# Kernel tuning notes

Hardware: AMD Instinct MI355X
Metric: run time of the kernel (lower is better)

## Reference

```python
import jax, jax.numpy as jnp
import numpy as np

B, D, H, NB = 16384, 1024, 256, 16

def setup_inputs() -> dict:
    key = jax.random.key(0)
    ks = jax.random.split(key, 10)
    s_d = 1.0 / np.sqrt(D)
    s_h = 1.0 / np.sqrt(H)
    return {
        "x":   jax.random.normal(ks[0], (B, D), jnp.float32),
        # switch: Linear(D,H) -> relu -> Linear(H, 3*NB)
        "Ws1": jax.random.normal(ks[1], (D, H), jnp.float32) * s_d,
        "bs1": jnp.zeros((H,), jnp.float32),
        "Ws2": jax.random.normal(ks[2], (H, 3 * NB), jnp.float32) * s_h,
        "bs2": jnp.zeros((3 * NB,), jnp.float32),
        # per-branch bottleneck FC operators: D -> H -> D
        "W1":  jax.random.normal(ks[3], (NB, D, H), jnp.float32) * s_d,
        "b1":  jnp.zeros((NB, H), jnp.float32),
        "W2":  jax.random.normal(ks[4], (NB, H, D), jnp.float32) * s_h,
        "b2":  jnp.zeros((NB, D), jnp.float32),
        # noise: uniform for gumbel, normal for reparameterized gaussian
        "u":   jax.random.uniform(ks[5], (B, NB), jnp.float32, 1e-6, 1.0 - 1e-6),
        "eps": jax.random.normal(ks[6], (B, NB), jnp.float32),
    }

def reference(x, Ws1, bs1, Ws2, bs2, W1, b1, W2, b2, u, eps):
    # switch -> control signals, reshaped to (B, 3, NB)
    ctrl = jax.nn.relu(x @ Ws1 + bs1) @ Ws2 + bs2
    ctrl = ctrl.reshape(-1, 3, NB)
    y_logits, z_mean, z_logvar = ctrl[:, 0], ctrl[:, 1], ctrl[:, 2]

    # gumbel-softmax sample (tau = 1)
    g = -jnp.log(-jnp.log(u))
    y = jax.nn.softmax(y_logits + g, axis=-1)          # soft sample (B, NB)
    y_idx = jnp.argmax(y, axis=-1)                     # hard branch per sample

    # gaussian reparameterization
    z = z_mean + jnp.exp(0.5 * z_logvar) * eps         # (B, NB)

    # per-branch bottleneck FC, z of the branch gates the bottleneck
    h = jax.nn.relu(jnp.einsum('bd,ndh->bnh', x, W1) + b1)   # (B, NB, H)
    h = h * z[:, :, None]
    o = jnp.einsum('bnh,nhd->bnd', h, W2) + b2               # (B, NB, D)

    # combine: keep only the branch selected by y_idx
    onehot = jax.nn.one_hot(y_idx, NB, dtype=x.dtype)        # (B, NB)
    out = jnp.einsum('bnd,bn->bd', o, onehot)                # (B, D)

    return (x + out, y_logits, y_idx, y, z_mean, z_logvar, z)
```

## Files before the change

### kernel.cpp

```cpp
#include <hip/hip_runtime.h>
#include <hip/hip_bf16.h>
#include <stdint.h>

#define Bn 16384
#define Dd 1024
#define Hh 256
#define NBk 16

#define O1 ((size_t)Bn*Dd)
#define O2 (O1 + (size_t)Bn*NBk)
#define O3 (O2 + (size_t)Bn)
#define O4 (O3 + (size_t)Bn*NBk)
#define O5 (O4 + (size_t)Bn*NBk)
#define O6 (O5 + (size_t)Bn*NBk)

typedef __attribute__((ext_vector_type(8))) short s16x8;
typedef __attribute__((ext_vector_type(4))) float f32x4;

#define MFMA_BF16(a,b,c) __builtin_amdgcn_mfma_f32_16x16x32_bf16((a),(b),(c),0,0,0)

__device__ __forceinline__ float blo(unsigned v){ return __uint_as_float(v << 16); }
__device__ __forceinline__ float bhi(unsigned v){ return __uint_as_float(v & 0xFFFF0000u); }
__device__ __forceinline__ unsigned short f2b(float f){
  unsigned u = __float_as_uint(f);
  return (unsigned short)((u + 0x7FFFu + ((u >> 16) & 1u)) >> 16);
}
__device__ __forceinline__ s16x8 cvt8(const f32x4 u0, const f32x4 u1) {
  s16x8 v;
  v[0]=(short)f2b(u0[0]); v[1]=(short)f2b(u0[1]); v[2]=(short)f2b(u0[2]); v[3]=(short)f2b(u0[3]);
  v[4]=(short)f2b(u1[0]); v[5]=(short)f2b(u1[1]); v[6]=(short)f2b(u1[2]); v[7]=(short)f2b(u1[3]);
  return v;
}
__device__ __forceinline__ void split8(const f32x4 u0, const f32x4 u1, s16x8& hi, s16x8& lo) {
  #pragma unroll
  for (int e = 0; e < 4; ++e) {
    const unsigned short h = f2b(u0[e]);
    hi[e] = (short)h;
    lo[e] = (short)f2b(u0[e] - __uint_as_float((unsigned)h << 16));
  }
  #pragma unroll
  for (int e = 0; e < 4; ++e) {
    const unsigned short h = f2b(u1[e]);
    hi[4+e] = (short)h;
    lo[4+e] = (short)f2b(u1[e] - __uint_as_float((unsigned)h << 16));
  }
}
__device__ __forceinline__ void gload16(const void* g, void* lds) {
  __builtin_amdgcn_global_load_lds(
      (const __attribute__((address_space(1))) unsigned int*)g,
      (__attribute__((address_space(3))) unsigned int*)lds, 16, 0, 0);
}

__global__ __launch_bounds__(256) void kA1(const float* __restrict__ x, const float* __restrict__ Ws1,
                                           const float* __restrict__ bs1, float* __restrict__ A1)
{
  const int b0 = blockIdx.x * 64;
  const int c0 = blockIdx.y * 128;
  __shared__ float XS[32][68];
  __shared__ float WS[32][128];
  const int tid = threadIdx.x;
  const int ty = tid >> 4, tx = tid & 15;
  float acc[4][8];
  #pragma unroll
  for (int r = 0; r < 4; ++r)
    #pragma unroll
    for (int c = 0; c < 8; ++c) acc[r][c] = 0.f;

  for (int k0 = 0; k0 < Dd; k0 += 32) {
    #pragma unroll
    for (int it = 0; it < 2; ++it) {
      int i = tid + 256*it;
      int row = i >> 3, kq = i & 7;
      float4 v = *(const float4*)&x[(size_t)(b0+row)*Dd + k0 + 4*kq];
      XS[4*kq+0][row] = v.x; XS[4*kq+1][row] = v.y; XS[4*kq+2][row] = v.z; XS[4*kq+3][row] = v.w;
    }
    #pragma unroll
    for (int it = 0; it < 4; ++it) {
      int i = tid + 256*it;
      int k = i >> 5, cq = i & 31;
      *(float4*)&WS[k][4*cq] = *(const float4*)&Ws1[(size_t)(k0+k)*Hh + c0 + 4*cq];
    }
    __syncthreads();
    #pragma unroll
    for (int k = 0; k < 32; ++k) {
      const float4 xv = *(const float4*)&XS[k][ty*4];
      const float4 w0 = *(const float4*)&WS[k][tx*4];
      const float4 w1 = *(const float4*)&WS[k][tx*4+64];
      const float xr[4] = {xv.x, xv.y, xv.z, xv.w};
      const float wr[8] = {w0.x,w0.y,w0.z,w0.w,w1.x,w1.y,w1.z,w1.w};
      #pragma unroll
      for (int r = 0; r < 4; ++r)
        #pragma unroll
        for (int c = 0; c < 8; ++c)
          acc[r][c] = fmaf(xr[r], wr[c], acc[r][c]);
    }
    __syncthreads();
  }
  const float4 bv0 = *(const float4*)&bs1[c0 + tx*4];
  const float4 bv1 = *(const float4*)&bs1[c0 + tx*4 + 64];
  const float br[8] = {bv0.x,bv0.y,bv0.z,bv0.w,bv1.x,bv1.y,bv1.z,bv1.w};
  #pragma unroll
  for (int r = 0; r < 4; ++r) {
    int row = b0 + ty*4 + r;
    float o[8];
    #pragma unroll
    for (int c = 0; c < 8; ++c) o[c] = fmaxf(acc[r][c] + br[c], 0.f);
    float4 s0 = {o[0],o[1],o[2],o[3]};
    float4 s1 = {o[4],o[5],o[6],o[7]};
    *(float4*)&A1[(size_t)row*Hh + c0 + tx*4]      = s0;
    *(float4*)&A1[(size_t)row*Hh + c0 + tx*4 + 64] = s1;
  }
}

__global__ __launch_bounds__(256) void kTW(const float* __restrict__ in,
                                           unsigned short* __restrict__ hi,
                                           unsigned short* __restrict__ lo)
{
  const int i0 = blockIdx.x * 32, j0 = blockIdx.y * 32;
  __shared__ float T[32][33];
  const int t = threadIdx.x;
  {
    const int ii = t >> 3, jj = (t & 7) * 4;
    float4 v = *(const float4*)&in[(size_t)(i0+ii)*Hh + j0 + jj];
    T[ii][jj] = v.x; T[ii][jj+1] = v.y; T[ii][jj+2] = v.z; T[ii][jj+3] = v.w;
  }
  __syncthreads();
  {
    const int jo = t >> 3, io = (t & 7) * 4;
    ushort4 sh, sl;
    float v0 = T[io+0][jo], v1 = T[io+1][jo], v2 = T[io+2][jo], v3 = T[io+3][jo];
    unsigned short h;
    h = f2b(v0); sh.x = h; sl.x = f2b(v0 - __uint_as_float((unsigned)h << 16));
    h = f2b(v1); sh.y = h; sl.y = f2b(v1 - __uint_as_float((unsigned)h << 16));
    h = f2b(v2); sh.z = h; sl.z = f2b(v2 - __uint_as_float((unsigned)h << 16));
    h = f2b(v3); sh.w = h; sl.w = f2b(v3 - __uint_as_float((unsigned)h << 16));
    *(ushort4*)&hi[(size_t)(j0+jo)*Dd + i0 + io] = sh;
    *(ushort4*)&lo[(size_t)(j0+jo)*Dd + i0 + io] = sl;
  }
}

__global__ __launch_bounds__(256) void kT2(const float* __restrict__ Ws2, float* __restrict__ Ws2T)
{
  const int j = blockIdx.x;
  const int k = threadIdx.x;
  Ws2T[(size_t)j * Hh + k] = Ws2[(size_t)k * 48 + j];
}

__global__ __launch_bounds__(256) void kA1s4(const float* __restrict__ x,
    const unsigned short* __restrict__ Whi, const unsigned short* __restrict__ Wlo,
    const float* __restrict__ bs1, float* __restrict__ A1)
{
  extern __shared__ __align__(16) char sm[];

  const int bid = blockIdx.x;
  const int b0 = (bid >> 1) * 32;
  const int cb = bid & 1;
  const int tid = threadIdx.x, l = tid & 63, w = tid >> 6;

  const int xrow = tid >> 3, xga = tid & 7;
  const int xdst = xrow * 128 + ((xga ^ (xrow & 7)) * 16);
  const size_t xsrc = (size_t)(b0 + xrow) * Dd + xga * 8;

  const unsigned short *hsrc[4], *lsrc[4];
  const unsigned short* Hbase = Whi + (size_t)(cb * 128) * Dd;
  const unsigned short* Lbase = Wlo + (size_t)(cb * 128) * Dd;
  #pragma unroll
  for (int t = 0; t < 4; ++t) {
    const int col = (w * 4 + t) * 8 + (l >> 3);
    const int sa = (l & 7) ^ (col & 7);
    hsrc[t] = Hbase + (size_t)col * Dd + sa * 8;
    lsrc[t] = Lbase + (size_t)col * Dd + sa * 8;
  }

  f32x4 acc[2][2];
  #pragma unroll
  for (int a = 0; a < 2; ++a)
    #pragma unroll
    for (int b_ = 0; b_ < 2; ++b_)
      #pragma unroll
      for (int e = 0; e < 4; ++e) acc[a][b_][e] = 0.f;

  f32x4 xa = *(const f32x4*)&x[xsrc];
  f32x4 xb = *(const f32x4*)&x[xsrc + 4];
  #pragma unroll
  for (int t = 0; t < 4; ++t) {
    gload16(hsrc[t], sm + 16384 + (w * 4 + t) * 1024);
    gload16(lsrc[t], sm + 16384 + 16384 + (w * 4 + t) * 1024);
  }
  {
    s16x8 hi8, lo8;
    split8(xa, xb, hi8, lo8);
    *(s16x8*)(sm + xdst) = hi8;
    *(s16x8*)(sm + 4096 + xdst) = lo8;
  }
  xa = *(const f32x4*)&x[xsrc + 64];
  xb = *(const f32x4*)&x[xsrc + 68];
  __syncthreads();

  for (int kc = 0; kc < 16; ++kc) {
    const char* Xb = sm + (kc & 1) * 8192;
    const char* Bb = sm + 16384 + (kc & 1) * 32768;

    if (kc < 15) {
      const int nb = (kc + 1) & 1;
      char* Bn_ = sm + 16384 + nb * 32768;
      #pragma unroll
      for (int t = 0; t < 4; ++t) {
        gload16(hsrc[t] + (kc + 1) * 64, Bn_ + (w * 4 + t) * 1024);
        gload16(lsrc[t] + (kc + 1) * 64, Bn_ + 16384 + (w * 4 + t) * 1024);
      }
      {
        s16x8 hi8, lo8;
        split8(xa, xb, hi8, lo8);
        *(s16x8*)(sm + nb * 8192 + xdst) = hi8;
        *(s16x8*)(sm + nb * 8192 + 4096 + xdst) = lo8;
      }
      if (kc < 14) {
        xa = *(const f32x4*)&x[xsrc + (kc + 2) * 64];
        xb = *(const f32x4*)&x[xsrc + (kc + 2) * 64 + 4];
      }
    }

    #pragma unroll
    for (int kk = 0; kk < 2; ++kk) {
      s16x8 ah[2], al[2], bh[2], bl[2];
      #pragma unroll
      for (int rf = 0; rf < 2; ++rf) {
        const int row = rf * 16 + (l & 15);
        const int g = (kk * 4 + (l >> 4)) ^ (row & 7);
        ah[rf] = *(const s16x8*)(Xb + row * 128 + g * 16);
        al[rf] = *(const s16x8*)(Xb + 4096 + row * 128 + g * 16);
      }
      #pragma unroll
      for (int cf = 0; cf < 2; ++cf) {
        const int col = w * 32 + cf * 16 + (l & 15);
        const int g = (kk * 4 + (l >> 4)) ^ (col & 7);
        bh[cf] = *(const s16x8*)(Bb + col * 128 + g * 16);
        bl[cf] = *(const s16x8*)(Bb + 16384 + col * 128 + g * 16);
      }
      #pragma unroll
      for (int rf = 0; rf < 2; ++rf)
        #pragma unroll
        for (int cf = 0; cf < 2; ++cf) {
          acc[rf][cf] = MFMA_BF16(ah[rf], bh[cf], acc[rf][cf]);
          acc[rf][cf] = MFMA_BF16(ah[rf], bl[cf], acc[rf][cf]);
          acc[rf][cf] = MFMA_BF16(al[rf], bh[cf], acc[rf][cf]);
        }
    }
    __syncthreads();
  }

  #pragma unroll
  for (int rf = 0; rf < 2; ++rf)
    #pragma unroll
    for (int cf = 0; cf < 2; ++cf)
      #pragma unroll
      for (int rg = 0; rg < 4; ++rg) {
        const int row = b0 + rf * 16 + (l >> 4) * 4 + rg;
        const int col = cb * 128 + w * 32 + cf * 16 + (l & 15);
        A1[(size_t)row * Hh + col] = fmaxf(acc[rf][cf][rg] + bs1[col], 0.f);
      }
}

__global__ __launch_bounds__(256) void kA2(const float* __restrict__ Ws2, const float* __restrict__ bs2,
                                           float* out)
{
  const int b0 = blockIdx.x * 64;
  __shared__ float XS[32][68];
  __shared__ float WC[32][48];
  const int tid = threadIdx.x;
  const int rg = tid >> 4, jg = tid & 15;
  float acc[4][3];
  #pragma unroll
  for (int r = 0; r < 4; ++r) { acc[r][0]=0.f; acc[r][1]=0.f; acc[r][2]=0.f; }
  const float* A1 = out;
  for (int kc = 0; kc < 8; ++kc) {
    const int k0 = kc*32;
    #pragma unroll
    for (int it = 0; it < 2; ++it) {
      int i = tid + 256*it;
      int row = i >> 3, kq = i & 7;
      float4 v = *(const float4*)&A1[(size_t)(b0+row)*Hh + k0 + 4*kq];
      XS[4*kq+0][row]=v.x; XS[4*kq+1][row]=v.y; XS[4*kq+2][row]=v.z; XS[4*kq+3][row]=v.w;
    }
    #pragma unroll
    for (int it = 0; it < 2; ++it) {
      int i = tid + 256*it;
      if (i < 384) {
        int k = i / 12, jq = i % 12;
        *(float4*)&WC[k][4*jq] = *(const float4*)&Ws2[(size_t)(k0+k)*48 + 4*jq];
      }
    }
    __syncthreads();
    #pragma unroll
    for (int k = 0; k < 32; ++k) {
      const float4 av = *(const float4*)&XS[k][rg*4];
      const float ar[4] = {av.x,av.y,av.z,av.w};
      const float w0 = WC[k][jg], w1 = WC[k][jg+16], w2 = WC[k][jg+32];
      #pragma unroll
      for (int r = 0; r < 4; ++r) {
        acc[r][0] = fmaf(ar[r], w0, acc[r][0]);
        acc[r][1] = fmaf(ar[r], w1, acc[r][1]);
        acc[r][2] = fmaf(ar[r], w2, acc[r][2]);
      }
    }
    __syncthreads();
  }
  const float c0b = bs2[jg], c1b = bs2[jg+16], c2b = bs2[jg+32];
  #pragma unroll
  for (int r = 0; r < 4; ++r) {
    size_t row = (size_t)b0 + rg*4 + r;
    out[O1 + row*NBk + jg] = acc[r][0] + c0b;
    out[O4 + row*NBk + jg] = acc[r][1] + c1b;
    out[O5 + row*NBk + jg] = acc[r][2] + c2b;
  }
}

__global__ __launch_bounds__(256) void kB2(const float* __restrict__ u, const float* __restrict__ eps,
                                           float* out, int* __restrict__ idxw, float* __restrict__ zsel,
                                           int* __restrict__ counts)
{
  const int e = blockIdx.x * 256 + threadIdx.x;
  const int b = e >> 4, j = e & 15;
  const float yl = out[O1 + e];
  const float zm = out[O4 + e];
  const float zv = out[O5 + e];
  const float s  = yl - logf(-logf(u[e]));
  const float z  = zm + expf(0.5f * zv) * eps[e];

  float bv = s; int bj = j;
  #pragma unroll
  for (int m = 8; m >= 1; m >>= 1) {
    const float ov = __shfl_xor(bv, m, 16);
    const int   oj = __shfl_xor(bj, m, 16);
    if (ov > bv || (ov == bv && oj < bj)) { bv = ov; bj = oj; }
  }
  const float ex = expf(s - bv);
  float sum = ex;
  #pragma unroll
  for (int m = 8; m >= 1; m >>= 1) sum += __shfl_xor(sum, m, 16);
  const float inv = 1.f / sum;

  out[O3 + e] = ex * inv;
  out[O6 + e] = z;
  if (j == bj) {
    out[O2 + b] = (float)bj;
    idxw[b] = bj;
    zsel[b] = z;
    atomicAdd(&counts[bj], 1);
  }
}

__global__ __launch_bounds__(256) void kB3(const float* __restrict__ A1, const float* __restrict__ Ws2T,
                                           const float* __restrict__ bs2,
                                           const float* __restrict__ u, const float* __restrict__ eps,
                                           float* out, int* __restrict__ idxw, float* __restrict__ zsel)
{
  __shared__ float AS[16][258];
  __shared__ float WS[48][258];
  const int tid = threadIdx.x;
  const int brow0 = blockIdx.x * 16;

  #pragma unroll
  for (int it = 0; it < 4; ++it) {
    const int i = tid + 256 * it;
    const int row = i >> 6, kq = i & 63;
    const f32x4 v = *(const f32x4*)&A1[(size_t)(brow0 + row) * Hh + kq * 4];
    *(f32x4*)&AS[row][kq * 4] = v;
  }
  #pragma unroll
  for (int it = 0; it < 12; ++it) {
    const int i = tid + 256 * it;
    const int row = i >> 6, kq = i & 63;
    const f32x4 v = *(const f32x4*)&Ws2T[(size_t)row * Hh + kq * 4];
    *(f32x4*)&WS[row][kq * 4] = v;
  }
  __syncthreads();

  const int e = blockIdx.x * 256 + tid;
  const int b = e >> 4, j = tid & 15;
  const int rl = tid >> 4;

  float c0 = 0.f, c1 = 0.f, c2 = 0.f;
  #pragma unroll 4
  for (int k = 0; k < Hh; k += 4) {
    const f32x4 av = *(const f32x4*)&AS[rl][k];
    const f32x4 wa = *(const f32x4*)&WS[j][k];
    const f32x4 wb = *(const f32x4*)&WS[j + 16][k];
    const f32x4 wc = *(const f32x4*)&WS[j + 32][k];
    #pragma unroll
    for (int kk = 0; kk < 4; ++kk) {
      c0 = fmaf(av[kk], wa[kk], c0);
      c1 = fmaf(av[kk], wb[kk], c1);
      c2 = fmaf(av[kk], wc[kk], c2);
    }
  }
  const float yl = c0 + bs2[j];
  const float zm = c1 + bs2[j + 16];
  const float zv = c2 + bs2[j + 32];

  const float s = yl - logf(-logf(u[e]));
  const float z = zm + expf(0.5f * zv) * eps[e];

  float bv = s; int bj = j;
  #pragma unroll
  for (int m = 8; m >= 1; m >>= 1) {
    const float ov = __shfl_xor(bv, m, 16);
    const int   oj = __shfl_xor(bj, m, 16);
    if (ov > bv || (ov == bv && oj < bj)) { bv = ov; bj = oj; }
  }
  const float ex = expf(s - bv);
  float sum = ex;
  #pragma unroll
  for (int m = 8; m >= 1; m >>= 1) sum += __shfl_xor(sum, m, 16);
  const float inv = 1.f / sum;

  out[O1 + e] = yl;
  out[O4 + e] = zm;
  out[O5 + e] = zv;
  out[O3 + e] = ex * inv;
  out[O6 + e] = z;
  if (j == bj) {
    out[O2 + b] = (float)bj;
    idxw[b] = bj;
    zsel[b] = z;
  }
}

__global__ __launch_bounds__(256) void kH(const int* __restrict__ idxw, int* __restrict__ counts)
{
  __shared__ int lh[NBk];
  const int tid = threadIdx.x;
  if (tid < NBk) lh[tid] = 0;
  __syncthreads();
  atomicAdd(&lh[idxw[blockIdx.x * 256 + tid]], 1);
  __syncthreads();
  if (tid < NBk && lh[tid]) atomicAdd(&counts[tid], lh[tid]);
}

__global__ void kP(const int* __restrict__ counts, int* __restrict__ offs, int* __restrict__ cursor,
                   int* __restrict__ bpre, int* __restrict__ tp1, int* __restrict__ tp2,
                   int* __restrict__ seg)
{
  if (threadIdx.x == 0 && blockIdx.x == 0) {
    int a = 0, bb = 0, t1 = 0, t2 = 0, sg = 0;
    for (int n = 0; n < NBk; ++n) {
      offs[n] = a; cursor[n] = a; bpre[n] = bb; tp1[n] = t1; tp2[n] = t2; seg[n] = sg;
      const int c = counts[n];
      a  += c;
      bb += (c + 31) >> 5;
      t1 += (c + 63) >> 6;
      t2 += (c + 127) >> 7;
      sg += ((c + 127) >> 7) * 128;
    }
    offs[NBk] = a; bpre[NBk] = bb; tp1[NBk] = t1; tp2[NBk] = t2; seg[NBk] = sg;
  }
}

__global__ __launch_bounds__(256) void kS(const int* __restrict__ idxw, int* __restrict__ cursor,
                                          int* __restrict__ rowlist)
{
  const int b = blockIdx.x * 256 + threadIdx.x;
  const int n = idxw[b];
  const int pos = atomicAdd(&cursor[n], 1);
  rowlist[pos] = b;
}

__global__ __launch_bounds__(256) void kS2(const int* __restrict__ idxw, int* __restrict__ cursor,
                                           int* __restrict__ rowlist)
{
  __shared__ int lh[NBk];
  __shared__ int gb[NBk];
  const int tid = threadIdx.x;
  const int b = blockIdx.x * 256 + tid;
  const int n = idxw[b];
  if (tid < NBk) lh[tid] = 0;
  __syncthreads();
  const int rank = atomicAdd(&lh[n], 1);
  __syncthreads();
  if (tid < NBk) gb[tid] = lh[tid] ? atomicAdd(&cursor[tid], lh[tid]) : 0;
  __syncthreads();
  rowlist[gb[n] + rank] = b;
}

__global__ __launch_bounds__(256) void kT(const float* __restrict__ in, unsigned short* __restrict__ out,
                                          int R, int C)
{
  const int n = blockIdx.z;
  in  += (size_t)n * R * C;
  out += (size_t)n * R * C;
  const int i0 = blockIdx.x * 32, j0 = blockIdx.y * 32;
  __shared__ float T[32][33];
  const int t = threadIdx.x;
  {
    const int ii = t >> 3, jj = (t & 7) * 4;
    float4 v = *(const float4*)&in[(size_t)(i0+ii)*C + j0 + jj];
    T[ii][jj] = v.x; T[ii][jj+1] = v.y; T[ii][jj+2] = v.z; T[ii][jj+3] = v.w;
  }
  __syncthreads();
  {
    const int jo = t >> 3, io = (t & 7) * 4;
    ushort4 st;
    st.x = f2b(T[io+0][jo]);
    st.y = f2b(T[io+1][jo]);
    st.z = f2b(T[io+2][jo]);
    st.w = f2b(T[io+3][jo]);
    *(ushort4*)&out[(size_t)(j0+jo)*R + i0 + io] = st;
  }
}

__global__ __launch_bounds__(256) void kG1(const float* __restrict__ x,
    const unsigned short* __restrict__ W1T, const float* __restrict__ b1,
    const int* __restrict__ rowlist, const float* __restrict__ zsel,
    const int* __restrict__ offs, const int* __restrict__ tp1, const int* __restrict__ seg,
    unsigned short* __restrict__ hbuf)
{
  __shared__ __align__(16) float Xs[64*64];
  __shared__ __align__(16) unsigned short Wsh[128*64];
  __shared__ int rows_s[64];
  __shared__ float zrs[64];

  const int bid = blockIdx.x;
  const int tile = bid >> 1, cb = bid & 1;
  if (tile >= tp1[NBk]) return;
  int n = 0;
  while (tile >= tp1[n+1]) ++n;
  const int tt = tile - tp1[n];
  const int base = offs[n], cnt = offs[n+1] - base;
  const int r0 = tt * 64;
  const int tid = threadIdx.x, l = tid & 63, w = tid >> 6;
  const int wr = w >> 1, wc = w & 1;

  if (tid < 64) {
    int r = r0 + tid;
    int g = rowlist[base + (r < cnt ? r : cnt - 1)];
    rows_s[tid] = g;
    zrs[tid] = zsel[g];
  }
  __syncthreads();

  size_t xsrc[4];
  const unsigned short* wsrc[4];
  const unsigned short* Wbase = W1T + (size_t)n * (Hh * Dd) + (size_t)(cb * 128) * Dd;
  #pragma unroll
  for (int t = 0; t < 4; ++t) {
    {
      int row = (w * 4 + t) * 4 + (l >> 4);
      int ga = (l & 15) ^ (row & 7);
      xsrc[t] = (size_t)rows_s[row] * Dd + ga * 4;
    }
    {
      int row = (w * 4 + t) * 8 + (l >> 3);
      int sa = (l & 7) ^ (row & 7);
      wsrc[t] = Wbase + (size_t)row * Dd + sa * 8;
    }
  }

  f32x4 acc[2][4];
  #pragma unroll
  for (int a = 0; a < 2; ++a)
    #pragma unroll
    for (int b_ = 0; b_ < 4; ++b_)
      #pragma unroll
      for (int e = 0; e < 4; ++e) acc[a][b_][e] = 0.f;

  for (int kc = 0; kc < 16; ++kc) {
    #pragma unroll
    for (int t = 0; t < 4; ++t) {
      gload16(&x[xsrc[t] + kc * 64], (char*)Xs + (w * 4 + t) * 1024);
      gload16(wsrc[t] + kc * 64, (char*)Wsh + (w * 4 + t) * 1024);
    }
    __syncthreads();

    #pragma unroll
    for (int kk = 0; kk < 2; ++kk) {
      s16x8 af[2], bf[4];
      #pragma unroll
      for (int rf = 0; rf < 2; ++rf) {
        const int row = wr * 32 + rf * 16 + (l & 15);
        const int gl = 8 * kk + 2 * (l >> 4);
        const int g0 = gl ^ (row & 7), g1 = (gl + 1) ^ (row & 7);
        f32x4 u0 = *(const f32x4*)((const char*)Xs + row * 256 + g0 * 16);
        f32x4 u1 = *(const f32x4*)((const char*)Xs + row * 256 + g1 * 16);
        af[rf] = cvt8(u0, u1);
      }
      #pragma unroll
      for (int cf = 0; cf < 4; ++cf) {
        const int col = wc * 64 + cf * 16 + (l & 15);
        const int s8 = (4 * kk + (l >> 4)) ^ (col & 7);
        bf[cf] = *(const s16x8*)((const char*)Wsh + col * 128 + s8 * 16);
      }
      #pragma unroll
      for (int rf = 0; rf < 2; ++rf)
        #pragma unroll
        for (int cf = 0; cf < 4; ++cf)
          acc[rf][cf] = MFMA_BF16(af[rf], bf[cf], acc[rf][cf]);
    }
    __syncthreads();
  }

  const size_t hrow0 = (size_t)seg[n] + r0;
  #pragma unroll
  for (int rf = 0; rf < 2; ++rf)
    #pragma unroll
    for (int cf = 0; cf < 4; ++cf)
      #pragma unroll
      for (int rg = 0; rg < 4; ++rg) {
        const int rloc = wr * 32 + rf * 16 + (l >> 4) * 4 + rg;
        const int col = cb * 128 + wc * 64 + cf * 16 + (l & 15);
        const float hv = fmaxf(acc[rf][cf][rg] + b1[n * Hh + col], 0.f) * zrs[rloc];
        hbuf[(hrow0 + rloc) * Hh + col] = f2b(hv);
      }
}

__global__ __launch_bounds__(256) void kG2(const float* __restrict__ x,
    const unsigned short* __restrict__ W2T, const float* __restrict__ b2,
    const unsigned short* __restrict__ hbuf, const int* __restrict__ rowlist,
    const int* __restrict__ offs, const int* __restrict__ tp2, const int* __restrict__ seg,
    float* __restrict__ out)
{
  __shared__ __align__(16) unsigned short As[128*64];
  __shared__ __align__(16) unsigned short Bs[128*64];
  __shared__ int rows_s[128];

  const int bid = blockIdx.x;
  const int tile = bid >> 3, cb = bid & 7;
  if (tile >= tp2[NBk]) return;
  int n = 0;
  while (tile >= tp2[n+1]) ++n;
  const int tt = tile - tp2[n];
  const int base = offs[n], cnt = offs[n+1] - base;
  const int r0 = tt * 128;
  const int tid = threadIdx.x, l = tid & 63, w = tid >> 6;
  const int wr = w >> 1, wc = w & 1;

  if (tid < 128) {
    int r = r0 + tid;
    rows_s[tid] = rowlist[base + (r < cnt ? r : cnt - 1)];
  }
  __syncthreads();

  const unsigned short* Abase = hbuf + (size_t)(seg[n] + r0) * Hh;
  const unsigned short* Bbase = W2T + (size_t)n * (Hh * Dd) + (size_t)(cb * 128) * Hh;

  const unsigned short* asrc[4];
  const unsigned short* bsrc[4];
  #pragma unroll
  for (int t = 0; t < 4; ++t) {
    const int row = (w * 4 + t) * 8 + (l >> 3);
    const int sa = (l & 7) ^ (row & 7);
    asrc[t] = Abase + (size_t)row * Hh + sa * 8;
    bsrc[t] = Bbase + (size_t)row * Hh + sa * 8;
  }

  f32x4 acc[4][4];
  #pragma unroll
  for (int a = 0; a < 4; ++a)
    #pragma unroll
    for (int b_ = 0; b_ < 4; ++b_)
      #pragma unroll
      for (int e = 0; e < 4; ++e) acc[a][b_][e] = 0.f;

  for (int kc = 0; kc < 4; ++kc) {
    #pragma unroll
    for (int t = 0; t < 4; ++t) {
      gload16(asrc[t] + kc * 64, (char*)As + (w * 4 + t) * 1024);
      gload16(bsrc[t] + kc * 64, (char*)Bs + (w * 4 + t) * 1024);
    }
    __syncthreads();

    #pragma unroll
    for (int kk = 0; kk < 2; ++kk) {
      s16x8 af[4], bf[4];
      #pragma unroll
      for (int rf = 0; rf < 4; ++rf) {
        const int row = wr * 64 + rf * 16 + (l & 15);
        const int s8 = (4 * kk + (l >> 4)) ^ (row & 7);
        af[rf] = *(const s16x8*)((const char*)As + row * 128 + s8 * 16);
      }
      #pragma unroll
      for (int cf = 0; cf < 4; ++cf) {
        const int col = wc * 64 + cf * 16 + (l & 15);
        const int s8 = (4 * kk + (l >> 4)) ^ (col & 7);
        bf[cf] = *(const s16x8*)((const char*)Bs + col * 128 + s8 * 16);
      }
      #pragma unroll
      for (int rf = 0; rf < 4; ++rf)
        #pragma unroll
        for (int cf = 0; cf < 4; ++cf)
          acc[rf][cf] = MFMA_BF16(af[rf], bf[cf], acc[rf][cf]);
    }
    __syncthreads();
  }

  #pragma unroll
  for (int rf = 0; rf < 4; ++rf)
    #pragma unroll
    for (int rg = 0; rg < 4; ++rg) {
      const int rloc = wr * 64 + rf * 16 + (l >> 4) * 4 + rg;
      if (r0 + rloc < cnt) {
        const int g = rows_s[rloc];
        #pragma unroll
        for (int cf = 0; cf < 4; ++cf) {
          const int col = cb * 128 + wc * 64 + cf * 16 + (l & 15);
          out[(size_t)g * Dd + col] = acc[rf][cf][rg] + b2[n * Dd + col] + x[(size_t)g * Dd + col];
        }
      }
    }
}

extern "C" void kernel_launch(void* const* d_in, const int* in_sizes, int n_in,
                              void* d_out, int out_size, void* d_ws, size_t ws_size,
                              hipStream_t stream) {
  const float* x   = (const float*)d_in[0];
  const float* Ws1 = (const float*)d_in[1];
  const float* bs1 = (const float*)d_in[2];
  const float* Ws2 = (const float*)d_in[3];
  const float* bs2 = (const float*)d_in[4];
  const float* W1  = (const float*)d_in[5];
  const float* b1  = (const float*)d_in[6];
  const float* W2  = (const float*)d_in[7];
  const float* b2  = (const float*)d_in[8];
  const float* u   = (const float*)d_in[9];
  const float* eps = (const float*)d_in[10];
  float* out = (float*)d_out;

  char* ws = (char*)d_ws;
  int*   counts  = (int*)(ws + 0);
  int*   cursor  = (int*)(ws + 64);
  int*   bpre    = (int*)(ws + 128);
  int*   offs    = (int*)(ws + 256);
  int*   tp1     = (int*)(ws + 384);
  int*   tp2     = (int*)(ws + 512);
  int*   seg     = (int*)(ws + 640);
  int*   idxw    = (int*)(ws + 4096);
  float* zsel    = (float*)(ws + 4096 + 65536);
  int*   rowlist = (int*)(ws + 4096 + 131072);
  float* Ws2T    = (float*)(ws + 786432);
  unsigned short* W1T  = (unsigned short*)(ws + ((size_t)1 << 20));
  unsigned short* W2T  = (unsigned short*)(ws + ((size_t)9 << 20));
  unsigned short* hbuf = (unsigned short*)(ws + ((size_t)17 << 20));
  unsigned short* Whi  = (unsigned short*)(ws + ((size_t)27 << 20));
  unsigned short* Wlo  = (unsigned short*)(ws + ((size_t)27 << 20) + (512<<10));

  const bool f2 = ws_size >= ((size_t)28 << 20);
  const bool f1 = ws_size >= ((size_t)18 << 20);

  hipMemsetAsync(d_ws, 0, 4096, stream);
  if (f1 || f2) {
    kT<<<dim3(32, 8, 16), 256, 0, stream>>>(W1, W1T, Dd, Hh);
    kT<<<dim3(8, 32, 16), 256, 0, stream>>>(W2, W2T, Hh, Dd);
  }
  if (f2) {
    kTW<<<dim3(32, 8), 256, 0, stream>>>(Ws1, Whi, Wlo);
    kT2<<<dim3(48), 256, 0, stream>>>(Ws2, Ws2T);
    kA1s4<<<dim3(1024), 256, 81920, stream>>>(x, Whi, Wlo, bs1, out);
    kB3<<<dim3(Bn/16), 256, 0, stream>>>(out, Ws2T, bs2, u, eps, out, idxw, zsel);
    kH <<<dim3(Bn/256), 256, 0, stream>>>(idxw, counts);
  } else {
    kA1<<<dim3(Bn/64, 2), 256, 0, stream>>>(x, Ws1, bs1, out);
    kA2<<<dim3(Bn/64), 256, 0, stream>>>(Ws2, bs2, out);
    kB2<<<dim3(Bn*NBk/256), 256, 0, stream>>>(u, eps, out, idxw, zsel, counts);
  }
  kP <<<dim3(1), 64, 0, stream>>>(counts, offs, cursor, bpre, tp1, tp2, seg);
  if (f2) {
    kS2<<<dim3(Bn/256), 256, 0, stream>>>(idxw, cursor, rowlist);
    kG1<<<dim3(544), 256, 0, stream>>>(x, W1T, b1, rowlist, zsel, offs, tp1, seg, hbuf);
    kG2<<<dim3(1152), 256, 0, stream>>>(x, W2T, b2, hbuf, rowlist, offs, tp2, seg, out);
  } else {
    kS<<<dim3(Bn/256), 256, 0, stream>>>(idxw, cursor, rowlist);
  }
}
```

Measured before the change: 169.2 us.

## Deepen prefetch pipeline in switch GEMM with explicit vmcnt waits and raw barriers

Restructures the first switch GEMM's main loop so weight tiles are prefetched two k-chunks ahead instead of one. Full __syncthreads are replaced by s_waitcnt with partial vmcnt counts plus s_barrier, so later loads stay in flight across the barrier. The last chunk is peeled into an epilogue. This aims to hide more global-load latency behind MFMA work. In exchange it relies on hand-counted outstanding loads, which are fragile, and the tail iterations issue redundant clamped loads.

```diff
diff --git a/kernel.cpp b/kernel.cpp
--- a/kernel.cpp
+++ b/kernel.cpp
@@ -146,7 +146,7 @@
   Ws2T[(size_t)j * Hh + k] = Ws2[(size_t)k * 48 + j];
 }
 
-__global__ __launch_bounds__(256) void kA1s4(const float* __restrict__ x,
+__global__ __launch_bounds__(256) void kA1s7(const float* __restrict__ x,
     const unsigned short* __restrict__ Whi, const unsigned short* __restrict__ Wlo,
     const float* __restrict__ bs1, float* __restrict__ A1)
 {
@@ -180,47 +180,45 @@
       #pragma unroll
       for (int e = 0; e < 4; ++e) acc[a][b_][e] = 0.f;
 
-  f32x4 xa = *(const f32x4*)&x[xsrc];
-  f32x4 xb = *(const f32x4*)&x[xsrc + 4];
+  f32x4 x0a = *(const f32x4*)&x[xsrc];
+  f32x4 x0b = *(const f32x4*)&x[xsrc + 4];
   #pragma unroll
   for (int t = 0; t < 4; ++t) {
     gload16(hsrc[t], sm + 16384 + (w * 4 + t) * 1024);
     gload16(lsrc[t], sm + 16384 + 16384 + (w * 4 + t) * 1024);
   }
+  f32x4 xa = *(const f32x4*)&x[xsrc + 64];
+  f32x4 xb = *(const f32x4*)&x[xsrc + 68];
+  #pragma unroll
+  for (int t = 0; t < 4; ++t) {
+    gload16(hsrc[t] + 64, sm + 16384 + 32768 + (w * 4 + t) * 1024);
+    gload16(lsrc[t] + 64, sm + 16384 + 32768 + 16384 + (w * 4 + t) * 1024);
+  }
   {
     s16x8 hi8, lo8;
-    split8(xa, xb, hi8, lo8);
+    split8(x0a, x0b, hi8, lo8);
     *(s16x8*)(sm + xdst) = hi8;
     *(s16x8*)(sm + 4096 + xdst) = lo8;
   }
-  xa = *(const f32x4*)&x[xsrc + 64];
-  xb = *(const f32x4*)&x[xsrc + 68];
-  __syncthreads();
-
-  for (int kc = 0; kc < 16; ++kc) {
-    const char* Xb = sm + (kc & 1) * 8192;
-    const char* Bb = sm + 16384 + (kc & 1) * 32768;
-
-    if (kc < 15) {
-      const int nb = (kc + 1) & 1;
-      char* Bn_ = sm + 16384 + nb * 32768;
-      #pragma unroll
-      for (int t = 0; t < 4; ++t) {
-        gload16(hsrc[t] + (kc + 1) * 64, Bn_ + (w * 4 + t) * 1024);
-        gload16(lsrc[t] + (kc + 1) * 64, Bn_ + 16384 + (w * 4 + t) * 1024);
-      }
-      {
-        s16x8 hi8, lo8;
-        split8(xa, xb, hi8, lo8);
-        *(s16x8*)(sm + nb * 8192 + xdst) = hi8;
-        *(s16x8*)(sm + nb * 8192 + 4096 + xdst) = lo8;
-      }
-      if (kc < 14) {
-        xa = *(const f32x4*)&x[xsrc + (kc + 2) * 64];
-        xb = *(const f32x4*)&x[xsrc + (kc + 2) * 64 + 4];
-      }
-    }
-
+  asm volatile("s_waitcnt vmcnt(10) lgkmcnt(0)" ::: "memory");
+  __builtin_amdgcn_s_barrier();
+
+  for (int kc = 0; kc < 15; ++kc) {
+    const int cur = kc & 1, nxt = cur ^ 1;
+    const char* Xb = sm + cur * 8192;
+    const char* Bb = sm + 16384 + cur * 32768;
+
+    {
+      s16x8 hi8, lo8;
+      split8(xa, xb, hi8, lo8);
+      *(s16x8*)(sm + nxt * 8192 + xdst) = hi8;
+      *(s16x8*)(sm + nxt * 8192 + 4096 + xdst) = lo8;
+    }
+    {
+      const int kn = kc + 2 < 16 ? kc + 2 : 15;
+      xa = *(const f32x4*)&x[xsrc + kn * 64];
+      xb = *(const f32x4*)&x[xsrc + kn * 64 + 4];
+    }
     #pragma unroll
     for (int kk = 0; kk < 2; ++kk) {
       s16x8 ah[2], al[2], bh[2], bl[2];
@@ -247,7 +245,48 @@
           acc[rf][cf] = MFMA_BF16(al[rf], bh[cf], acc[rf][cf]);
         }
     }
-    __syncthreads();
+    asm volatile("s_waitcnt vmcnt(2) lgkmcnt(0)" ::: "memory");
+    __builtin_amdgcn_s_barrier();
+    {
+      const int kn = kc + 2 < 16 ? kc + 2 : 15;
+      char* Wd = sm + 16384 + cur * 32768;
+      #pragma unroll
+      for (int t = 0; t < 4; ++t) {
+        gload16(hsrc[t] + kn * 64, Wd + (w * 4 + t) * 1024);
+        gload16(lsrc[t] + kn * 64, Wd + 16384 + (w * 4 + t) * 1024);
+      }
+    }
+  }
+
+  {
+    const char* Xb = sm + 8192;
+    const char* Bb = sm + 16384 + 32768;
+    #pragma unroll
+    for (int kk = 0; kk < 2; ++kk) {
+      s16x8 ah[2], al[2], bh[2], bl[2];
+      #pragma unroll
+      for (int rf = 0; rf < 2; ++rf) {
+        const int row = rf * 16 + (l & 15);
+        const int g = (kk * 4 + (l >> 4)) ^ (row & 7);
+        ah[rf] = *(const s16x8*)(Xb + row * 128 + g * 16);
+        al[rf] = *(const s16x8*)(Xb + 4096 + row * 128 + g * 16);
+      }
+      #pragma unroll
+      for (int cf = 0; cf < 2; ++cf) {
+        const int col = w * 32 + cf * 16 + (l & 15);
+        const int g = (kk * 4 + (l >> 4)) ^ (col & 7);
+        bh[cf] = *(const s16x8*)(Bb + col * 128 + g * 16);
+        bl[cf] = *(const s16x8*)(Bb + 16384 + col * 128 + g * 16);
+      }
+      #pragma unroll
+      for (int rf = 0; rf < 2; ++rf)
+        #pragma unroll
+        for (int cf = 0; cf < 2; ++cf) {
+          acc[rf][cf] = MFMA_BF16(ah[rf], bh[cf], acc[rf][cf]);
+          acc[rf][cf] = MFMA_BF16(ah[rf], bl[cf], acc[rf][cf]);
+          acc[rf][cf] = MFMA_BF16(al[rf], bh[cf], acc[rf][cf]);
+        }
+    }
   }
 
   #pragma unroll
@@ -754,7 +793,7 @@
   if (f2) {
     kTW<<<dim3(32, 8), 256, 0, stream>>>(Ws1, Whi, Wlo);
     kT2<<<dim3(48), 256, 0, stream>>>(Ws2, Ws2T);
-    kA1s4<<<dim3(1024), 256, 81920, stream>>>(x, Whi, Wlo, bs1, out);
+    kA1s7<<<dim3(1024), 256, 81920, stream>>>(x, Whi, Wlo, bs1, out);
     kB3<<<dim3(Bn/16), 256, 0, stream>>>(out, Ws2T, bs2, u, eps, out, idxw, zsel);
     kH <<<dim3(Bn/256), 256, 0, stream>>>(idxw, counts);
   } else {
```

Measured after the change: 174.3 us. 1.03x slower.
